# Optimization experiments

Measured on AMD Instinct MI355X. Metric: run time of the kernel, lower is better.

The kernel has to match this reference:

```python
import jax, jax.numpy as jnp
import numpy as np

N_MELS = 80
LSTM_DIM = 1024
ATT_DIM = 128
ENC_DIM = 512
PRENET = 256
LOC_FILT = 32
LOC_K = 31


def _lstm_step(x, h, c, k, r, b):
    z = x @ k + h @ r + b  # [B, 4*LSTM_DIM], keras gate order i,f,g,o
    i, f, g, o = jnp.split(z, 4, axis=-1)
    c2 = jax.nn.sigmoid(f) * c + jax.nn.sigmoid(i) * jnp.tanh(g)
    h2 = jax.nn.sigmoid(o) * jnp.tanh(c2)
    return h2, c2


def setup_inputs() -> dict:
    key = jax.random.key(0)
    ks = jax.random.split(key, 24)
    s = 0.05
    B, Tm, T = 32, 200, 400
    inp = {
        'memory': jax.random.normal(ks[0], (B, Tm, ENC_DIM), jnp.float32),
        'decoder_inputs': jax.random.normal(ks[1], (B, N_MELS, T), jnp.float32),
        # Prenet (2 dense+relu layers)
        'prenet_w0': jax.random.normal(ks[2], (N_MELS, PRENET)) * s,
        'prenet_b0': jnp.zeros((PRENET,)),
        'prenet_w1': jax.random.normal(ks[3], (PRENET, PRENET)) * s,
        'prenet_b1': jnp.zeros((PRENET,)),
        # LSTM 1: input = prenet(256) + context(512) = 768
        'lstm1_k': jax.random.normal(ks[4], (PRENET + ENC_DIM, 4 * LSTM_DIM)) * s,
        'lstm1_r': jax.random.normal(ks[5], (LSTM_DIM, 4 * LSTM_DIM)) * s,
        'lstm1_b': jnp.zeros((4 * LSTM_DIM,)),
        # LSTM 2: input = att_hidden(1024) + context(512) = 1536
        'lstm2_k': jax.random.normal(ks[6], (LSTM_DIM + ENC_DIM, 4 * LSTM_DIM)) * s,
        'lstm2_r': jax.random.normal(ks[7], (LSTM_DIM, 4 * LSTM_DIM)) * s,
        'lstm2_b': jnp.zeros((4 * LSTM_DIM,)),
        # Attention
        'wq': jax.random.normal(ks[8], (LSTM_DIM, ATT_DIM)) * s,
        'wm': jax.random.normal(ks[9], (ENC_DIM, ATT_DIM)) * s,
        'v': jax.random.normal(ks[10], (ATT_DIM,)) * s,
        'loc_conv': jax.random.normal(ks[11], (LOC_K, 2, LOC_FILT)) * s,  # WIO
        'loc_dense': jax.random.normal(ks[12], (LOC_FILT, ATT_DIM)) * s,
        # Projections: input = dec_hidden(1024) + context(512) = 1536
        'frame_w': jax.random.normal(ks[13], (LSTM_DIM + ENC_DIM, N_MELS)) * s,
        'frame_b': jnp.zeros((N_MELS,)),
        'stop_w': jax.random.normal(ks[14], (LSTM_DIM + ENC_DIM, 1)) * s,
        'stop_b': jnp.zeros((1,)),
    }
    return inp


def reference(memory, decoder_inputs, prenet_w0, prenet_b0, prenet_w1, prenet_b1,
              lstm1_k, lstm1_r, lstm1_b, lstm2_k, lstm2_r, lstm2_b,
              wq, wm, v, loc_conv, loc_dense, frame_w, frame_b, stop_w, stop_b):
    B, Tm, _ = memory.shape
    T = decoder_inputs.shape[2]

    # parse_decoder_inputs: [B, n_mels, T] -> [T, B, n_mels]; prepend go frame
    dec_in = jnp.transpose(decoder_inputs, (2, 0, 1))
    dec_in = jnp.concatenate([jnp.zeros((1, B, N_MELS), memory.dtype), dec_in], axis=0)
    # Prenet (dropout identity in inference mode)
    x = jax.nn.relu(dec_in @ prenet_w0 + prenet_b0)
    x = jax.nn.relu(x @ prenet_w1 + prenet_b1)  # [T+1, B, 256]

    processed_memory = jnp.tanh(memory @ wm)  # [B, Tm, ATT_DIM]

    def step(carry, xt):
        att_h, att_c, dec_h, dec_c, att_w, att_w_cum, att_ctx = carry
        # Attention RNN
        cell_in = jnp.concatenate([xt, att_ctx], axis=-1)
        att_h, att_c = _lstm_step(cell_in, att_h, att_c, lstm1_k, lstm1_r, lstm1_b)
        # Location-sensitive attention
        awc = jnp.stack([att_w, att_w_cum], axis=-1)  # [B, Tm, 2]
        loc = jax.lax.conv_general_dilated(awc, loc_conv, (1,), 'SAME',
                                           dimension_numbers=('NWC', 'WIO', 'NWC'))
        loc = jnp.tanh(loc @ loc_dense)  # [B, Tm, ATT_DIM]
        q = jnp.tanh(att_h @ wq)[:, None, :]  # [B, 1, ATT_DIM]
        energies = jnp.tanh(q + loc + processed_memory) @ v  # [B, Tm]
        att_w = jax.nn.softmax(energies, axis=1)
        att_ctx = jnp.einsum('bt,btd->bd', att_w, memory)  # [B, ENC_DIM]
        att_w_cum = att_w_cum + att_w
        # Decoder RNN
        dec_in2 = jnp.concatenate([att_h, att_ctx], axis=-1)
        dec_h, dec_c = _lstm_step(dec_in2, dec_h, dec_c, lstm2_k, lstm2_r, lstm2_b)
        dhac = jnp.concatenate([dec_h, att_ctx], axis=-1)
        mel = dhac @ frame_w + frame_b  # [B, n_mels]
        gate = jax.nn.sigmoid(dhac @ stop_w + stop_b)[:, 0]  # [B]
        carry = (att_h, att_c, dec_h, dec_c, att_w, att_w_cum, att_ctx)
        return carry, (mel, gate, att_w)

    z = jnp.zeros((B, LSTM_DIM), memory.dtype)
    zw = jnp.zeros((B, Tm), memory.dtype)
    zc = jnp.zeros((B, ENC_DIM), memory.dtype)
    carry0 = (z, z, z, z, zw, zw, zc)
    _, (mels, gates, aligns) = jax.lax.scan(step, carry0, x[:T])

    # parse_decoder_outputs
    mel_outputs = jnp.transpose(mels, (1, 2, 0))      # [B, n_mels, T]
    gate_outputs = jnp.transpose(gates, (1, 0))       # [B, T]
    alignments = jnp.transpose(aligns, (1, 0, 2))     # [B, T, Tm]
    return mel_outputs, gate_outputs, alignments
```

## Files before the change

### kernel.cpp

```cpp
#include <hip/hip_runtime.h>
#include <math.h>

#define TSTEPS 400

#define KSP1 7
#define KSP2 8

#define OFF_XPRE  0u
#define OFF_PM    1638400u
#define OFF_IN1T  2457600u
#define OFF_IN2T  2506752u
#define OFF_ZP1   2588672u
#define OFF_ZP2   3506176u
#define OFF_CTXP  4554752u
#define OFF_H2B   4620288u
#define OFF_C1    4685824u
#define OFF_C2    4718592u
#define OFF_ATTW  4751360u
#define OFF_CUM   4757760u
#define WS_FLOATS 4764160u

#define OUT_GATE  1024000
#define OUT_ALIGN 1036800

__device__ __forceinline__ float sigf(float x)   { return 1.f / (1.f + __expf(-x)); }
__device__ __forceinline__ float tanhf_(float x) { return 1.f - 2.f / (__expf(2.f*x) + 1.f); }

__global__ void __launch_bounds__(256) prenet_kernel(
    const float* __restrict__ dec, const float* __restrict__ w0, const float* __restrict__ b0,
    const float* __restrict__ w1, const float* __restrict__ b1, float* __restrict__ ws)
{
    __shared__ float s_in[80];
    __shared__ float s_h0[256];
    int t = blockIdx.x, b = blockIdx.y, tid = threadIdx.x;
    if (tid < 80) s_in[tid] = (t == 0) ? 0.f : dec[b*32000 + tid*400 + (t-1)];
    __syncthreads();
    float s = b0[tid];
    for (int m = 0; m < 80; ++m) s = fmaf(s_in[m], w0[m*256 + tid], s);
    s_h0[tid] = fmaxf(s, 0.f);
    __syncthreads();
    float s2 = b1[tid];
    for (int k = 0; k < 256; ++k) s2 = fmaf(s_h0[k], w1[k*256 + tid], s2);
    float v = fmaxf(s2, 0.f);
    unsigned u = __float_as_uint(v);
    u += 0x7fffu + ((u >> 16) & 1u);
    ((unsigned short*)(ws + OFF_XPRE))[(size_t)t*8192 + tid*32 + b] = (unsigned short)(u >> 16);
}

__global__ void __launch_bounds__(128) pmem_kernel(
    const float* __restrict__ mp, const float* __restrict__ wm, float* __restrict__ ws)
{
    int t = blockIdx.x, b = blockIdx.y, a = threadIdx.x;
    const float* mrow = mp + (b*200 + t)*512;
    float s = 0.f;
    for (int d = 0; d < 512; ++d) s = fmaf(mrow[d], wm[d*128 + a], s);
    ws[OFF_PM + (b*200 + t)*128 + a] = tanhf_(s);
}

__global__ void __launch_bounds__(256) zero_kernel(float* __restrict__ ws)
{
    int gid = blockIdx.x*256 + threadIdx.x, gsz = gridDim.x*256;
    for (int i = gid; i < 49152; i += gsz) ws[OFF_IN1T + i] = 0.f;
    for (int i = gid; i < 81920; i += gsz) ws[OFF_IN2T + i] = 0.f;
    for (int i = gid; i < 32768; i += gsz) { ws[OFF_C1 + i] = 0.f; ws[OFF_C2 + i] = 0.f; }
    for (int i = gid; i < 65536; i += gsz) { ws[OFF_CTXP + i] = 0.f; ws[OFF_H2B + i] = 0.f; }
    for (int i = gid; i < 6400;  i += gsz) { ws[OFF_ATTW + i] = 0.f; ws[OFF_CUM + i] = 0.f; }
}

#define FMA8(XA, XB, W)                                                                               \
    a[0].x = fmaf(XA.x, W.x, a[0].x); a[0].y = fmaf(XA.x, W.y, a[0].y); a[0].z = fmaf(XA.x, W.z, a[0].z); a[0].w = fmaf(XA.x, W.w, a[0].w); \
    a[1].x = fmaf(XA.y, W.x, a[1].x); a[1].y = fmaf(XA.y, W.y, a[1].y); a[1].z = fmaf(XA.y, W.z, a[1].z); a[1].w = fmaf(XA.y, W.w, a[1].w); \
    a[2].x = fmaf(XA.z, W.x, a[2].x); a[2].y = fmaf(XA.z, W.y, a[2].y); a[2].z = fmaf(XA.z, W.z, a[2].z); a[2].w = fmaf(XA.z, W.w, a[2].w); \
    a[3].x = fmaf(XA.w, W.x, a[3].x); a[3].y = fmaf(XA.w, W.y, a[3].y); a[3].z = fmaf(XA.w, W.z, a[3].z); a[3].w = fmaf(XA.w, W.w, a[3].w); \
    a[4].x = fmaf(XB.x, W.x, a[4].x); a[4].y = fmaf(XB.x, W.y, a[4].y); a[4].z = fmaf(XB.x, W.z, a[4].z); a[4].w = fmaf(XB.x, W.w, a[4].w); \
    a[5].x = fmaf(XB.y, W.x, a[5].x); a[5].y = fmaf(XB.y, W.y, a[5].y); a[5].z = fmaf(XB.y, W.z, a[5].z); a[5].w = fmaf(XB.y, W.w, a[5].w); \
    a[6].x = fmaf(XB.z, W.x, a[6].x); a[6].y = fmaf(XB.z, W.y, a[6].y); a[6].z = fmaf(XB.z, W.z, a[6].z); a[6].w = fmaf(XB.z, W.w, a[6].w); \
    a[7].x = fmaf(XB.w, W.x, a[7].x); a[7].y = fmaf(XB.w, W.y, a[7].y); a[7].z = fmaf(XB.w, W.z, a[7].z); a[7].w = fmaf(XB.w, W.w, a[7].w)

__global__ void __launch_bounds__(512, 4) kernel_P1(
    const float* __restrict__ l1k, const float* __restrict__ l1r,
    const float* __restrict__ l2k, const float* __restrict__ l2r,
    float* __restrict__ ws, int t)
{
    __shared__ float s_lds[12288];
    const int tid = threadIdx.x, bid = blockIdx.x;
    const int jq = tid & 31, bgrp = (tid >> 5) & 3, ksub = tid >> 7;
    const int b0 = bgrp*8;
    float4 a[8];
#pragma unroll
    for (int i = 0; i < 8; ++i) a[i] = make_float4(0.f, 0.f, 0.f, 0.f);

    if (bid < 224) {
        if (t >= TSTEPS) return;
        const int colgrp = bid & 31, ksp = bid >> 5;
        const int j = colgrp*128 + jq*4;

        if (ksp == 0) {
            const uint4* src = (const uint4*)((const unsigned short*)(ws + OFF_XPRE) + (size_t)t*8192);
            for (int i = tid; i < 1024; i += 512) {
                uint4 p = src[i];
                float* d = s_lds + i*8;
                d[0] = __uint_as_float(p.x << 16); d[1] = __uint_as_float(p.x & 0xffff0000u);
                d[2] = __uint_as_float(p.y << 16); d[3] = __uint_as_float(p.y & 0xffff0000u);
                d[4] = __uint_as_float(p.z << 16); d[5] = __uint_as_float(p.z & 0xffff0000u);
                d[6] = __uint_as_float(p.w << 16); d[7] = __uint_as_float(p.w & 0xffff0000u);
            }
        } else {
            const float4* src = (const float4*)(ws + OFF_IN1T - 8192 + (size_t)ksp*256*32);
            float4* dst = (float4*)s_lds;
            for (int i = tid; i < 2048; i += 512) dst[i] = src[i];
        }
        __syncthreads();

        const int kl0 = ksub*64;
        const int kg0 = ksp*256 + kl0;
        const float* wb = (kg0 < 768) ? (l1k + (size_t)kg0*4096 + j)
                                      : (l1r + (size_t)(kg0 - 768)*4096 + j);
        float4 wbuf[4];
#pragma unroll
        for (int i = 0; i < 4; ++i) wbuf[i] = *(const float4*)(wb + (size_t)i*4096);
        for (int kk = 0; kk < 60; kk += 4) {
            float4 wn[4];
#pragma unroll
            for (int i = 0; i < 4; ++i) wn[i] = *(const float4*)(wb + (size_t)(kk + 4 + i)*4096);
#pragma unroll
            for (int i = 0; i < 4; ++i) {
                const float* xp = s_lds + (kl0 + kk + i)*32 + b0;
                float4 xa = *(const float4*)xp;
                float4 xb = *(const float4*)(xp + 4);
                FMA8(xa, xb, wbuf[i]);
            }
#pragma unroll
            for (int i = 0; i < 4; ++i) wbuf[i] = wn[i];
        }
#pragma unroll
        for (int i = 0; i < 4; ++i) {
            const float* xp = s_lds + (kl0 + 60 + i)*32 + b0;
            float4 xa = *(const float4*)xp;
            float4 xb = *(const float4*)(xp + 4);
            FMA8(xa, xb, wbuf[i]);
        }

        __syncthreads();
        if (ksub) {
#pragma unroll
            for (int i = 0; i < 8; ++i)
                *(float4*)(s_lds + (ksub-1)*4096 + (b0 + i)*128 + jq*4) = a[i];
        }
        __syncthreads();
        if (!ksub) {
            float* zp1 = ws + OFF_ZP1;
#pragma unroll
            for (int i = 0; i < 8; ++i) {
                float4 r0 = *(const float4*)(s_lds +         (b0 + i)*128 + jq*4);
                float4 r1 = *(const float4*)(s_lds +  4096 + (b0 + i)*128 + jq*4);
                float4 r2 = *(const float4*)(s_lds +  8192 + (b0 + i)*128 + jq*4);
                a[i].x += r0.x + r1.x + r2.x; a[i].y += r0.y + r1.y + r2.y;
                a[i].z += r0.z + r1.z + r2.z; a[i].w += r0.w + r1.w + r2.w;
                *(float4*)(zp1 + (size_t)(ksp*32 + b0 + i)*4096 + j) = a[i];
            }
        }
    } else {
        if (t < 1 || t > TSTEPS) return;
        const int g = bid - 224;
        const int colgrp = g & 31, ksp = g >> 5;
        const int j = colgrp*128 + jq*4;

        {
            const float4* src = (const float4*)(ws + OFF_IN2T + (size_t)ksp*320*32);
            float4* dst = (float4*)s_lds;
            for (int i = tid; i < 2560; i += 512) dst[i] = src[i];
        }
        __syncthreads();

        const int kl0 = ksub*80;
        const int kg0 = ksp*320 + kl0;
        float4 wbuf[4];
#pragma unroll
        for (int i = 0; i < 4; ++i) {
            int kg = kg0 + i;
            const float* wr = (kg < 1536) ? (l2k + (size_t)kg*4096)
                                          : (l2r + (size_t)(kg - 1536)*4096);
            wbuf[i] = *(const float4*)(wr + j);
        }
        for (int kk = 0; kk < 76; kk += 4) {
            float4 wn[4];
#pragma unroll
            for (int i = 0; i < 4; ++i) {
                int kg = kg0 + kk + 4 + i;
                const float* wr = (kg < 1536) ? (l2k + (size_t)kg*4096)
                                              : (l2r + (size_t)(kg - 1536)*4096);
                wn[i] = *(const float4*)(wr + j);
            }
#pragma unroll
            for (int i = 0; i < 4; ++i) {
                const float* xp = s_lds + (kl0 + kk + i)*32 + b0;
                float4 xa = *(const float4*)xp;
                float4 xb = *(const float4*)(xp + 4);
                FMA8(xa, xb, wbuf[i]);
            }
#pragma unroll
            for (int i = 0; i < 4; ++i) wbuf[i] = wn[i];
        }
#pragma unroll
        for (int i = 0; i < 4; ++i) {
            const float* xp = s_lds + (kl0 + 76 + i)*32 + b0;
            float4 xa = *(const float4*)xp;
            float4 xb = *(const float4*)(xp + 4);
            FMA8(xa, xb, wbuf[i]);
        }

        __syncthreads();
        if (ksub) {
#pragma unroll
            for (int i = 0; i < 8; ++i)
                *(float4*)(s_lds + (ksub-1)*4096 + (b0 + i)*128 + jq*4) = a[i];
        }
        __syncthreads();
        if (!ksub) {
            float* zp2 = ws + OFF_ZP2;
#pragma unroll
            for (int i = 0; i < 8; ++i) {
                float4 r0 = *(const float4*)(s_lds +         (b0 + i)*128 + jq*4);
                float4 r1 = *(const float4*)(s_lds +  4096 + (b0 + i)*128 + jq*4);
                float4 r2 = *(const float4*)(s_lds +  8192 + (b0 + i)*128 + jq*4);
                a[i].x += r0.x + r1.x + r2.x; a[i].y += r0.y + r1.y + r2.y;
                a[i].z += r0.z + r1.z + r2.z; a[i].w += r0.w + r1.w + r2.w;
                *(float4*)(zp2 + (size_t)(ksp*32 + b0 + i)*4096 + j) = a[i];
            }
        }
    }
}

__global__ void __launch_bounds__(1024) kernel_P2(
    const float* __restrict__ mp, const float* __restrict__ l1b, const float* __restrict__ l2b,
    const float* __restrict__ wq, const float* __restrict__ vvec,
    const float* __restrict__ lconv, const float* __restrict__ ldense,
    const float* __restrict__ fw, const float* __restrict__ fb,
    const float* __restrict__ sw, const float* __restrict__ sb,
    float* __restrict__ ws, float* __restrict__ out, int t)
{
    __shared__ float s_attw[200], s_cum[200];
    __shared__ float s_hid[1024], s_q[128], s_ex[200], s_den[1];
    __shared__ float s_co[200*33];
    __shared__ float s_red[1024];
    const int tid = threadIdx.x, bid = blockIdx.x;
    float* in1m = ws + OFF_IN1T - 8192;
    float* in2T = ws + OFF_IN2T;
    float* zp1  = ws + OFF_ZP1;
    float* zp2  = ws + OFF_ZP2;
    float* ctxp = ws + OFF_CTXP;
    float* h2bb = ws + OFF_H2B;
    float* c1a  = ws + OFF_C1;
    float* c2a  = ws + OFF_C2;
    float* attw = ws + OFF_ATTW;
    float* cum  = ws + OFF_CUM;
    const float* pm = ws + OFF_PM;

    if (bid < 32) {
        if (t >= TSTEPS) return;
        const int b = bid;
        {
            int u = tid;
            float zi = l1b[u], zf = l1b[1024+u], zg = l1b[2048+u], zo = l1b[3072+u];
#pragma unroll
            for (int kc = 0; kc < KSP1; ++kc) {
                const float* zr = zp1 + (size_t)(kc*32 + b)*4096;
                zi += zr[u]; zf += zr[1024+u]; zg += zr[2048+u]; zo += zr[3072+u];
            }
            float c = sigf(zf)*c1a[b*1024+u] + sigf(zi)*tanhf_(zg);
            float h = sigf(zo)*tanhf_(c);
            c1a[b*1024+u] = c;
            s_hid[u] = h;
            in1m[(768+u)*32 + b] = h;
            in2T[u*32 + b] = h;
        }
        if (tid < 200) { s_attw[tid] = attw[b*200 + tid]; s_cum[tid] = cum[b*200 + tid]; }
        __syncthreads();
        {
            int a = tid & 127, kq = tid >> 7;
            float s = 0.f;
            for (int k = kq*128; k < kq*128 + 128; ++k)
                s = fmaf(s_hid[k], wq[k*128 + a], s);
            s_red[tid] = s;
        }
        __syncthreads();
        if (tid < 128) {
            float s = 0.f;
#pragma unroll
            for (int q = 0; q < 8; ++q) s += s_red[q*128 + tid];
            s_q[tid] = tanhf_(s);
        }
        for (int idx = tid; idx < 6400; idx += 1024) {
            int tl = idx >> 5, f = idx & 31;
            float s = 0.f;
            for (int dw = 0; dw < 31; ++dw) {
                int tg = tl - 15 + dw;
                if (tg >= 0 && tg < 200) {
                    s = fmaf(s_attw[tg], lconv[(dw*2+0)*32 + f], s);
                    s = fmaf(s_cum[tg],  lconv[(dw*2+1)*32 + f], s);
                }
            }
            s_co[tl*33 + f] = s;
        }
        __syncthreads();
        if (tid < 800) {
            int tl = tid >> 2, aq = tid & 3;
            const float* pmrow = pm + (b*200 + tl)*128;
            float e = 0.f;
            for (int a = aq*32; a < aq*32 + 32; ++a) {
                float s = 0.f;
#pragma unroll
                for (int f = 0; f < 32; ++f) s = fmaf(s_co[tl*33 + f], ldense[f*128 + a], s);
                float en = tanhf_(s_q[a] + tanhf_(s) + pmrow[a]);
                e = fmaf(en, vvec[a], e);
            }
            e += __shfl_xor(e, 1, 4);
            e += __shfl_xor(e, 2, 4);
            if (aq == 0) s_ex[tl] = __expf(e);
        }
        __syncthreads();
        if (tid < 64) {
            float s = 0.f;
            for (int i = tid; i < 200; i += 64) s += s_ex[i];
            for (int off = 32; off; off >>= 1) s += __shfl_down(s, off, 64);
            if (tid == 0) s_den[0] = s;
        }
        __syncthreads();
        if (tid < 200) {
            float w = s_ex[tid] / s_den[0];
            s_attw[tid] = w;
            attw[b*200 + tid] = w;
            cum[b*200 + tid] = s_cum[tid] + w;
            out[OUT_ALIGN + (b*400 + t)*200 + tid] = w;
        }
        __syncthreads();
        {
            int d = tid & 511, th = tid >> 9;
            float s = 0.f;
            for (int tt = th*100; tt < th*100 + 100; ++tt)
                s = fmaf(s_attw[tt], mp[(b*200 + tt)*512 + d], s);
            s_red[tid] = s;
        }
        __syncthreads();
        if (tid < 512) {
            float cv = s_red[tid] + s_red[512 + tid];
            ctxp[(size_t)(t & 3)*16384 + b*512 + tid] = cv;
            in1m[(256 + tid)*32 + b] = cv;
            in2T[(1024 + tid)*32 + b] = cv;
        }
    } else if (bid < 64) {
        if (t < 1 || t > TSTEPS) return;
        const int b = bid - 32, t1 = t - 1;
        float* h2b = h2bb + (size_t)(t1 & 1)*32768;
        int u = tid;
        float zi = l2b[u], zf = l2b[1024+u], zg = l2b[2048+u], zo = l2b[3072+u];
#pragma unroll
        for (int kc = 0; kc < KSP2; ++kc) {
            const float* zr = zp2 + (size_t)(kc*32 + b)*4096;
            zi += zr[u]; zf += zr[1024+u]; zg += zr[2048+u]; zo += zr[3072+u];
        }
        float c = sigf(zf)*c2a[b*1024+u] + sigf(zi)*tanhf_(zg);
        float h = sigf(zo)*tanhf_(c);
        c2a[b*1024+u] = c;
        in2T[(1536+u)*32 + b] = h;
        h2b[u*32 + b] = h;
    } else if (bid < 74) {
        if (t < 2) return;
        const int t2 = t - 2;
        const int mc = bid - 64;
        const int m_l = tid & 7, b = (tid >> 3) & 31, kh = tid >> 8;
        const int m = mc*8 + m_l;
        const float* cp = ctxp + (size_t)((t2 & 3)*32 + b)*512;
        const float* h2b = h2bb + (size_t)(t2 & 1)*32768;
        float s = 0.f;
        for (int k = kh*384; k < kh*384 + 384; ++k) {
            float dv = (k < 1024) ? h2b[k*32 + b] : cp[k - 1024];
            s = fmaf(dv, fw[k*80 + m], s);
        }
        s_red[tid] = s;
        __syncthreads();
        if (tid < 256) {
            float v4 = s_red[tid] + s_red[256+tid] + s_red[512+tid] + s_red[768+tid];
            int b2 = tid >> 3, m2 = mc*8 + (tid & 7);
            out[(b2*80 + m2)*400 + t2] = v4 + fb[m2];
        }
    } else {
        if (t < 2) return;
        const int t2 = t - 2;
        const int b = tid >> 5, kh = tid & 31;
        const float* cp = ctxp + (size_t)((t2 & 3)*32 + b)*512;
        const float* h2b = h2bb + (size_t)(t2 & 1)*32768;
        float s = 0.f;
        for (int k = kh*48; k < kh*48 + 48; ++k) {
            float dv = (k < 1024) ? h2b[k*32 + b] : cp[k - 1024];
            s = fmaf(dv, sw[k], s);
        }
        s_red[b*32 + kh] = s;
        __syncthreads();
        if (tid < 32) {
            float z = 0.f;
#pragma unroll
            for (int i = 0; i < 32; ++i) z += s_red[tid*32 + i];
            out[OUT_GATE + tid*400 + t2] = sigf(z + sb[0]);
        }
    }
}

extern "C" void kernel_launch(void* const* d_in, const int* in_sizes, int n_in,
                              void* d_out, int out_size, void* d_ws, size_t ws_size,
                              hipStream_t stream) {
    (void)in_sizes; (void)n_in; (void)out_size;
    const float* mp    = (const float*)d_in[0];
    const float* dec   = (const float*)d_in[1];
    const float* pw0   = (const float*)d_in[2];
    const float* pb0   = (const float*)d_in[3];
    const float* pw1   = (const float*)d_in[4];
    const float* pb1   = (const float*)d_in[5];
    const float* l1k   = (const float*)d_in[6];
    const float* l1r   = (const float*)d_in[7];
    const float* l1b   = (const float*)d_in[8];
    const float* l2k   = (const float*)d_in[9];
    const float* l2r   = (const float*)d_in[10];
    const float* l2b   = (const float*)d_in[11];
    const float* wq    = (const float*)d_in[12];
    const float* wm    = (const float*)d_in[13];
    const float* vvec  = (const float*)d_in[14];
    const float* lconv = (const float*)d_in[15];
    const float* ldns  = (const float*)d_in[16];
    const float* fw    = (const float*)d_in[17];
    const float* fb    = (const float*)d_in[18];
    const float* sw    = (const float*)d_in[19];
    const float* sb    = (const float*)d_in[20];
    float* ws  = (float*)d_ws;
    float* out = (float*)d_out;

    if (ws_size < (size_t)WS_FLOATS * sizeof(float)) return;

    prenet_kernel<<<dim3(400, 32), 256, 0, stream>>>(dec, pw0, pb0, pw1, pb1, ws);
    pmem_kernel  <<<dim3(200, 32), 128, 0, stream>>>(mp, wm, ws);
    zero_kernel  <<<256, 256, 0, stream>>>(ws);

    for (int t = 0; t <= TSTEPS; ++t) {
        kernel_P1<<<480, 512, 0, stream>>>(l1k, l1r, l2k, l2r, ws, t);
        kernel_P2<<<75, 1024, 0, stream>>>(mp, l1b, l2b, wq, vvec, lconv, ldns,
                                           fw, fb, sw, sb, ws, out, t);
    }
    kernel_P2<<<75, 1024, 0, stream>>>(mp, l1b, l2b, wq, vvec, lconv, ldns,
                                       fw, fb, sw, sb, ws, out, TSTEPS + 1);
}
```

Baseline: 75.90 ms.

## Move mel/gate projections into P1 and rebalance GEMM k-split per thread

Moves the frame and stop projections out of the serial attention/LSTM kernel P2 and into the wide P1 kernel as extra blocks, so they run alongside the LSTM gate GEMMs and P2 becomes shorter on the critical path. The P1 GEMM is reorganised from a 4-way k-split with 8 batch rows per thread to a 2-way k-split with 4 batch rows and 8-deep weight prefetch, which shrinks the LDS reduction and changes register pressure. It also adds unroll pragmas to several P2 loops. The projection blocks now run at step t in P1 instead of after P2, which depends on buffer parity timing staying correct.

After: 110.3 ms. +45.3%, slower.

```diff
diff --git a/kernel.cpp b/kernel.cpp
--- a/kernel.cpp
+++ b/kernel.cpp
@@ -67,167 +67,197 @@
     for (int i = gid; i < 6400;  i += gsz) { ws[OFF_ATTW + i] = 0.f; ws[OFF_CUM + i] = 0.f; }
 }
 
-#define FMA8(XA, XB, W)                                                                               \
-    a[0].x = fmaf(XA.x, W.x, a[0].x); a[0].y = fmaf(XA.x, W.y, a[0].y); a[0].z = fmaf(XA.x, W.z, a[0].z); a[0].w = fmaf(XA.x, W.w, a[0].w); \
-    a[1].x = fmaf(XA.y, W.x, a[1].x); a[1].y = fmaf(XA.y, W.y, a[1].y); a[1].z = fmaf(XA.y, W.z, a[1].z); a[1].w = fmaf(XA.y, W.w, a[1].w); \
-    a[2].x = fmaf(XA.z, W.x, a[2].x); a[2].y = fmaf(XA.z, W.y, a[2].y); a[2].z = fmaf(XA.z, W.z, a[2].z); a[2].w = fmaf(XA.z, W.w, a[2].w); \
-    a[3].x = fmaf(XA.w, W.x, a[3].x); a[3].y = fmaf(XA.w, W.y, a[3].y); a[3].z = fmaf(XA.w, W.z, a[3].z); a[3].w = fmaf(XA.w, W.w, a[3].w); \
-    a[4].x = fmaf(XB.x, W.x, a[4].x); a[4].y = fmaf(XB.x, W.y, a[4].y); a[4].z = fmaf(XB.x, W.z, a[4].z); a[4].w = fmaf(XB.x, W.w, a[4].w); \
-    a[5].x = fmaf(XB.y, W.x, a[5].x); a[5].y = fmaf(XB.y, W.y, a[5].y); a[5].z = fmaf(XB.y, W.z, a[5].z); a[5].w = fmaf(XB.y, W.w, a[5].w); \
-    a[6].x = fmaf(XB.z, W.x, a[6].x); a[6].y = fmaf(XB.z, W.y, a[6].y); a[6].z = fmaf(XB.z, W.z, a[6].z); a[6].w = fmaf(XB.z, W.w, a[6].w); \
-    a[7].x = fmaf(XB.w, W.x, a[7].x); a[7].y = fmaf(XB.w, W.y, a[7].y); a[7].z = fmaf(XB.w, W.z, a[7].z); a[7].w = fmaf(XB.w, W.w, a[7].w)
+#define FMA4(X, W)                                                                                    \
+    a[0].x = fmaf(X.x, W.x, a[0].x); a[0].y = fmaf(X.x, W.y, a[0].y); a[0].z = fmaf(X.x, W.z, a[0].z); a[0].w = fmaf(X.x, W.w, a[0].w); \
+    a[1].x = fmaf(X.y, W.x, a[1].x); a[1].y = fmaf(X.y, W.y, a[1].y); a[1].z = fmaf(X.y, W.z, a[1].z); a[1].w = fmaf(X.y, W.w, a[1].w); \
+    a[2].x = fmaf(X.z, W.x, a[2].x); a[2].y = fmaf(X.z, W.y, a[2].y); a[2].z = fmaf(X.z, W.z, a[2].z); a[2].w = fmaf(X.z, W.w, a[2].w); \
+    a[3].x = fmaf(X.w, W.x, a[3].x); a[3].y = fmaf(X.w, W.y, a[3].y); a[3].z = fmaf(X.w, W.z, a[3].z); a[3].w = fmaf(X.w, W.w, a[3].w)
 
 __global__ void __launch_bounds__(512, 4) kernel_P1(
     const float* __restrict__ l1k, const float* __restrict__ l1r,
     const float* __restrict__ l2k, const float* __restrict__ l2r,
-    float* __restrict__ ws, int t)
+    const float* __restrict__ fw, const float* __restrict__ fb,
+    const float* __restrict__ sw, const float* __restrict__ sb,
+    float* __restrict__ ws, float* __restrict__ out, int t)
 {
-    __shared__ float s_lds[12288];
+    __shared__ float s_lds[10240];
     const int tid = threadIdx.x, bid = blockIdx.x;
-    const int jq = tid & 31, bgrp = (tid >> 5) & 3, ksub = tid >> 7;
-    const int b0 = bgrp*8;
-    float4 a[8];
-#pragma unroll
-    for (int i = 0; i < 8; ++i) a[i] = make_float4(0.f, 0.f, 0.f, 0.f);
-
-    if (bid < 224) {
-        if (t >= TSTEPS) return;
-        const int colgrp = bid & 31, ksp = bid >> 5;
-        const int j = colgrp*128 + jq*4;
-
-        if (ksp == 0) {
-            const uint4* src = (const uint4*)((const unsigned short*)(ws + OFF_XPRE) + (size_t)t*8192);
-            for (int i = tid; i < 1024; i += 512) {
-                uint4 p = src[i];
-                float* d = s_lds + i*8;
-                d[0] = __uint_as_float(p.x << 16); d[1] = __uint_as_float(p.x & 0xffff0000u);
-                d[2] = __uint_as_float(p.y << 16); d[3] = __uint_as_float(p.y & 0xffff0000u);
-                d[4] = __uint_as_float(p.z << 16); d[5] = __uint_as_float(p.z & 0xffff0000u);
-                d[6] = __uint_as_float(p.w << 16); d[7] = __uint_as_float(p.w & 0xffff0000u);
+
+    if (bid < 480) {
+        const int jq = tid & 31, bgrp = (tid >> 5) & 7, ksub = tid >> 8;
+        const int b0 = bgrp*4;
+        float4 a[4];
+#pragma unroll
+        for (int i = 0; i < 4; ++i) a[i] = make_float4(0.f, 0.f, 0.f, 0.f);
+
+        if (bid < 224) {
+            if (t >= TSTEPS) return;
+            const int colgrp = bid & 31, ksp = bid >> 5;
+            const int j = colgrp*128 + jq*4;
+
+            if (ksp == 0) {
+                const uint4* src = (const uint4*)((const unsigned short*)(ws + OFF_XPRE) + (size_t)t*8192);
+                for (int i = tid; i < 1024; i += 512) {
+                    uint4 p = src[i];
+                    float* d = s_lds + i*8;
+                    d[0] = __uint_as_float(p.x << 16); d[1] = __uint_as_float(p.x & 0xffff0000u);
+                    d[2] = __uint_as_float(p.y << 16); d[3] = __uint_as_float(p.y & 0xffff0000u);
+                    d[4] = __uint_as_float(p.z << 16); d[5] = __uint_as_float(p.z & 0xffff0000u);
+                    d[6] = __uint_as_float(p.w << 16); d[7] = __uint_as_float(p.w & 0xffff0000u);
+                }
+            } else {
+                const float4* src = (const float4*)(ws + OFF_IN1T - 8192 + (size_t)ksp*256*32);
+                float4* dst = (float4*)s_lds;
+                for (int i = tid; i < 2048; i += 512) dst[i] = src[i];
+            }
+            __syncthreads();
+
+            const int kl0 = ksub*128;
+            const int kg0 = ksp*256 + kl0;
+            const float* wb = (ksp < 3) ? (l1k + (size_t)kg0*4096 + j)
+                                        : (l1r + (size_t)(kg0 - 768)*4096 + j);
+            const float* xb = s_lds + kl0*32 + b0;
+            float4 wc[8], wn[8];
+#pragma unroll
+            for (int i = 0; i < 8; ++i) wc[i] = *(const float4*)(wb + (size_t)i*4096);
+            for (int kk = 0; kk < 120; kk += 8) {
+#pragma unroll
+                for (int i = 0; i < 8; ++i) wn[i] = *(const float4*)(wb + (size_t)(kk + 8 + i)*4096);
+#pragma unroll
+                for (int i = 0; i < 8; ++i) {
+                    float4 x = *(const float4*)(xb + (kk + i)*32);
+                    FMA4(x, wc[i]);
+                }
+#pragma unroll
+                for (int i = 0; i < 8; ++i) wc[i] = wn[i];
+            }
+#pragma unroll
+            for (int i = 0; i < 8; ++i) {
+                float4 x = *(const float4*)(xb + (120 + i)*32);
+                FMA4(x, wc[i]);
+            }
+
+            __syncthreads();
+            if (ksub) {
+#pragma unroll
+                for (int i = 0; i < 4; ++i)
+                    *(float4*)(s_lds + (b0 + i)*128 + jq*4) = a[i];
+            }
+            __syncthreads();
+            if (!ksub) {
+                float* zp1 = ws + OFF_ZP1;
+#pragma unroll
+                for (int i = 0; i < 4; ++i) {
+                    float4 r = *(const float4*)(s_lds + (b0 + i)*128 + jq*4);
+                    a[i].x += r.x; a[i].y += r.y; a[i].z += r.z; a[i].w += r.w;
+                    *(float4*)(zp1 + (size_t)(ksp*32 + b0 + i)*4096 + j) = a[i];
+                }
             }
         } else {
-            const float4* src = (const float4*)(ws + OFF_IN1T - 8192 + (size_t)ksp*256*32);
-            float4* dst = (float4*)s_lds;
-            for (int i = tid; i < 2048; i += 512) dst[i] = src[i];
-        }
-        __syncthreads();
-
-        const int kl0 = ksub*64;
-        const int kg0 = ksp*256 + kl0;
-        const float* wb = (kg0 < 768) ? (l1k + (size_t)kg0*4096 + j)
-                                      : (l1r + (size_t)(kg0 - 768)*4096 + j);
-        float4 wbuf[4];
-#pragma unroll
-        for (int i = 0; i < 4; ++i) wbuf[i] = *(const float4*)(wb + (size_t)i*4096);
-        for (int kk = 0; kk < 60; kk += 4) {
-            float4 wn[4];
-#pragma unroll
-            for (int i = 0; i < 4; ++i) wn[i] = *(const float4*)(wb + (size_t)(kk + 4 + i)*4096);
-#pragma unroll
-            for (int i = 0; i < 4; ++i) {
-                const float* xp = s_lds + (kl0 + kk + i)*32 + b0;
-                float4 xa = *(const float4*)xp;
-                float4 xb = *(const float4*)(xp + 4);
-                FMA8(xa, xb, wbuf[i]);
-            }
-#pragma unroll
-            for (int i = 0; i < 4; ++i) wbuf[i] = wn[i];
-        }
-#pragma unroll
-        for (int i = 0; i < 4; ++i) {
-            const float* xp = s_lds + (kl0 + 60 + i)*32 + b0;
-            float4 xa = *(const float4*)xp;
-            float4 xb = *(const float4*)(xp + 4);
-            FMA8(xa, xb, wbuf[i]);
-        }
-
-        __syncthreads();
-        if (ksub) {
-#pragma unroll
-            for (int i = 0; i < 8; ++i)
-                *(float4*)(s_lds + (ksub-1)*4096 + (b0 + i)*128 + jq*4) = a[i];
-        }
-        __syncthreads();
-        if (!ksub) {
-            float* zp1 = ws + OFF_ZP1;
+            if (t < 1 || t > TSTEPS) return;
+            const int g = bid - 224;
+            const int colgrp = g & 31, ksp = g >> 5;
+            const int j = colgrp*128 + jq*4;
+
+            {
+                const float4* src = (const float4*)(ws + OFF_IN2T + (size_t)ksp*320*32);
+                float4* dst = (float4*)s_lds;
+                for (int i = tid; i < 2560; i += 512) dst[i] = src[i];
+            }
+            __syncthreads();
+
+            const int kl0 = ksub*160;
+            const int kg0 = ksp*320 + kl0;
+            const float* xb = s_lds + kl0*32 + b0;
+            float4 wc[8], wn[8];
 #pragma unroll
             for (int i = 0; i < 8; ++i) {
-                float4 r0 = *(const float4*)(s_lds +         (b0 + i)*128 + jq*4);
-                float4 r1 = *(const float4*)(s_lds +  4096 + (b0 + i)*128 + jq*4);
-                float4 r2 = *(const float4*)(s_lds +  8192 + (b0 + i)*128 + jq*4);
-                a[i].x += r0.x + r1.x + r2.x; a[i].y += r0.y + r1.y + r2.y;
-                a[i].z += r0.z + r1.z + r2.z; a[i].w += r0.w + r1.w + r2.w;
-                *(float4*)(zp1 + (size_t)(ksp*32 + b0 + i)*4096 + j) = a[i];
-            }
-        }
-    } else {
-        if (t < 1 || t > TSTEPS) return;
-        const int g = bid - 224;
-        const int colgrp = g & 31, ksp = g >> 5;
-        const int j = colgrp*128 + jq*4;
-
-        {
-            const float4* src = (const float4*)(ws + OFF_IN2T + (size_t)ksp*320*32);
-            float4* dst = (float4*)s_lds;
-            for (int i = tid; i < 2560; i += 512) dst[i] = src[i];
-        }
-        __syncthreads();
-
-        const int kl0 = ksub*80;
-        const int kg0 = ksp*320 + kl0;
-        float4 wbuf[4];
-#pragma unroll
-        for (int i = 0; i < 4; ++i) {
-            int kg = kg0 + i;
-            const float* wr = (kg < 1536) ? (l2k + (size_t)kg*4096)
-                                          : (l2r + (size_t)(kg - 1536)*4096);
-            wbuf[i] = *(const float4*)(wr + j);
-        }
-        for (int kk = 0; kk < 76; kk += 4) {
-            float4 wn[4];
-#pragma unroll
-            for (int i = 0; i < 4; ++i) {
-                int kg = kg0 + kk + 4 + i;
+                int kg = kg0 + i;
                 const float* wr = (kg < 1536) ? (l2k + (size_t)kg*4096)
                                               : (l2r + (size_t)(kg - 1536)*4096);
-                wn[i] = *(const float4*)(wr + j);
-            }
-#pragma unroll
-            for (int i = 0; i < 4; ++i) {
-                const float* xp = s_lds + (kl0 + kk + i)*32 + b0;
-                float4 xa = *(const float4*)xp;
-                float4 xb = *(const float4*)(xp + 4);
-                FMA8(xa, xb, wbuf[i]);
-            }
-#pragma unroll
-            for (int i = 0; i < 4; ++i) wbuf[i] = wn[i];
-        }
-#pragma unroll
-        for (int i = 0; i < 4; ++i) {
-            const float* xp = s_lds + (kl0 + 76 + i)*32 + b0;
-            float4 xa = *(const float4*)xp;
-            float4 xb = *(const float4*)(xp + 4);
-            FMA8(xa, xb, wbuf[i]);
-        }
-
-        __syncthreads();
-        if (ksub) {
-#pragma unroll
-            for (int i = 0; i < 8; ++i)
-                *(float4*)(s_lds + (ksub-1)*4096 + (b0 + i)*128 + jq*4) = a[i];
-        }
-        __syncthreads();
-        if (!ksub) {
-            float* zp2 = ws + OFF_ZP2;
+                wc[i] = *(const float4*)(wr + j);
+            }
+            for (int kk = 0; kk < 152; kk += 8) {
+#pragma unroll
+                for (int i = 0; i < 8; ++i) {
+                    int kg = kg0 + kk + 8 + i;
+                    const float* wr = (kg < 1536) ? (l2k + (size_t)kg*4096)
+                                                  : (l2r + (size_t)(kg - 1536)*4096);
+                    wn[i] = *(const float4*)(wr + j);
+                }
+#pragma unroll
+                for (int i = 0; i < 8; ++i) {
+                    float4 x = *(const float4*)(xb + (kk + i)*32);
+                    FMA4(x, wc[i]);
+                }
+#pragma unroll
+                for (int i = 0; i < 8; ++i) wc[i] = wn[i];
+            }
 #pragma unroll
             for (int i = 0; i < 8; ++i) {
-                float4 r0 = *(const float4*)(s_lds +         (b0 + i)*128 + jq*4);
-                float4 r1 = *(const float4*)(s_lds +  4096 + (b0 + i)*128 + jq*4);
-                float4 r2 = *(const float4*)(s_lds +  8192 + (b0 + i)*128 + jq*4);
-                a[i].x += r0.x + r1.x + r2.x; a[i].y += r0.y + r1.y + r2.y;
-                a[i].z += r0.z + r1.z + r2.z; a[i].w += r0.w + r1.w + r2.w;
-                *(float4*)(zp2 + (size_t)(ksp*32 + b0 + i)*4096 + j) = a[i];
-            }
+                float4 x = *(const float4*)(xb + (152 + i)*32);
+                FMA4(x, wc[i]);
+            }
+
+            __syncthreads();
+            if (ksub) {
+#pragma unroll
+                for (int i = 0; i < 4; ++i)
+                    *(float4*)(s_lds + (b0 + i)*128 + jq*4) = a[i];
+            }
+            __syncthreads();
+            if (!ksub) {
+                float* zp2 = ws + OFF_ZP2;
+#pragma unroll
+                for (int i = 0; i < 4; ++i) {
+                    float4 r = *(const float4*)(s_lds + (b0 + i)*128 + jq*4);
+                    a[i].x += r.x; a[i].y += r.y; a[i].z += r.z; a[i].w += r.w;
+                    *(float4*)(zp2 + (size_t)(ksp*32 + b0 + i)*4096 + j) = a[i];
+                }
+            }
+        }
+    } else if (bid < 520) {
+        if (t < 2 || t > TSTEPS + 1) return;
+        const int t2 = t - 2;
+        const int mc = bid - 480;
+        const int m_l = tid & 1, b = (tid >> 1) & 31, kh = tid >> 6;
+        const int m = mc*2 + m_l;
+        const float* cp  = ws + OFF_CTXP + (size_t)((t2 & 3)*32 + b)*512;
+        const float* h2b = ws + OFF_H2B + (size_t)(t2 & 1)*32768;
+        float s = 0.f;
+#pragma unroll 8
+        for (int k = kh*192; k < kh*192 + 192; ++k) {
+            float dv = (k < 1024) ? h2b[k*32 + b] : cp[k - 1024];
+            s = fmaf(dv, fw[k*80 + m], s);
+        }
+        s_lds[tid] = s;
+        __syncthreads();
+        if (tid < 64) {
+            float v = 0.f;
+#pragma unroll
+            for (int kh2 = 0; kh2 < 8; ++kh2) v += s_lds[kh2*64 + tid];
+            int b2 = tid >> 1, m2 = mc*2 + (tid & 1);
+            out[(b2*80 + m2)*400 + t2] = v + fb[m2];
+        }
+    } else {
+        if (t < 2 || t > TSTEPS + 1) return;
+        const int t2 = t - 2;
+        const int b = tid >> 4, kh = tid & 15;
+        const float* cp  = ws + OFF_CTXP + (size_t)((t2 & 3)*32 + b)*512;
+        const float* h2b = ws + OFF_H2B + (size_t)(t2 & 1)*32768;
+        float s = 0.f;
+#pragma unroll 8
+        for (int k = kh*96; k < kh*96 + 96; ++k) {
+            float dv = (k < 1024) ? h2b[k*32 + b] : cp[k - 1024];
+            s = fmaf(dv, sw[k], s);
+        }
+        s_lds[tid] = s;
+        __syncthreads();
+        if (tid < 32) {
+            float z = 0.f;
+#pragma unroll
+            for (int i = 0; i < 16; ++i) z += s_lds[tid*16 + i];
+            out[OUT_GATE + tid*400 + t2] = sigf(z + sb[0]);
         }
     }
 }
@@ -236,8 +266,6 @@
     const float* __restrict__ mp, const float* __restrict__ l1b, const float* __restrict__ l2b,
     const float* __restrict__ wq, const float* __restrict__ vvec,
     const float* __restrict__ lconv, const float* __restrict__ ldense,
-    const float* __restrict__ fw, const float* __restrict__ fb,
-    const float* __restrict__ sw, const float* __restrict__ sb,
     float* __restrict__ ws, float* __restrict__ out, int t)
 {
     __shared__ float s_attw[200], s_cum[200];
@@ -280,6 +308,7 @@
         {
             int a = tid & 127, kq = tid >> 7;
             float s = 0.f;
+#pragma unroll 8
             for (int k = kq*128; k < kq*128 + 128; ++k)
                 s = fmaf(s_hid[k], wq[k*128 + a], s);
             s_red[tid] = s;
@@ -308,6 +337,7 @@
             int tl = tid >> 2, aq = tid & 3;
             const float* pmrow = pm + (b*200 + tl)*128;
             float e = 0.f;
+#pragma unroll 2
             for (int a = aq*32; a < aq*32 + 32; ++a) {
                 float s = 0.f;
 #pragma unroll
@@ -338,6 +368,7 @@
         {
             int d = tid & 511, th = tid >> 9;
             float s = 0.f;
+#pragma unroll 10
             for (int tt = th*100; tt < th*100 + 100; ++tt)
                 s = fmaf(s_attw[tt], mp[(b*200 + tt)*512 + d], s);
             s_red[tid] = s;
@@ -349,7 +380,7 @@
             in1m[(256 + tid)*32 + b] = cv;
             in2T[(1024 + tid)*32 + b] = cv;
         }
-    } else if (bid < 64) {
+    } else {
         if (t < 1 || t > TSTEPS) return;
         const int b = bid - 32, t1 = t - 1;
         float* h2b = h2bb + (size_t)(t1 & 1)*32768;
@@ -365,45 +396,6 @@
         c2a[b*1024+u] = c;
         in2T[(1536+u)*32 + b] = h;
         h2b[u*32 + b] = h;
-    } else if (bid < 74) {
-        if (t < 2) return;
-        const int t2 = t - 2;
-        const int mc = bid - 64;
-        const int m_l = tid & 7, b = (tid >> 3) & 31, kh = tid >> 8;
-        const int m = mc*8 + m_l;
-        const float* cp = ctxp + (size_t)((t2 & 3)*32 + b)*512;
-        const float* h2b = h2bb + (size_t)(t2 & 1)*32768;
-        float s = 0.f;
-        for (int k = kh*384; k < kh*384 + 384; ++k) {
-            float dv = (k < 1024) ? h2b[k*32 + b] : cp[k - 1024];
-            s = fmaf(dv, fw[k*80 + m], s);
-        }
-        s_red[tid] = s;
-        __syncthreads();
-        if (tid < 256) {
-            float v4 = s_red[tid] + s_red[256+tid] + s_red[512+tid] + s_red[768+tid];
-            int b2 = tid >> 3, m2 = mc*8 + (tid & 7);
-            out[(b2*80 + m2)*400 + t2] = v4 + fb[m2];
-        }
-    } else {
-        if (t < 2) return;
-        const int t2 = t - 2;
-        const int b = tid >> 5, kh = tid & 31;
-        const float* cp = ctxp + (size_t)((t2 & 3)*32 + b)*512;
-        const float* h2b = h2bb + (size_t)(t2 & 1)*32768;
-        float s = 0.f;
-        for (int k = kh*48; k < kh*48 + 48; ++k) {
-            float dv = (k < 1024) ? h2b[k*32 + b] : cp[k - 1024];
-            s = fmaf(dv, sw[k], s);
-        }
-        s_red[b*32 + kh] = s;
-        __syncthreads();
-        if (tid < 32) {
-            float z = 0.f;
-#pragma unroll
-            for (int i = 0; i < 32; ++i) z += s_red[tid*32 + i];
-            out[OUT_GATE + tid*400 + t2] = sigf(z + sb[0]);
-        }
     }
 }
 
@@ -442,10 +434,8 @@
     zero_kernel  <<<256, 256, 0, stream>>>(ws);
 
     for (int t = 0; t <= TSTEPS; ++t) {
-        kernel_P1<<<480, 512, 0, stream>>>(l1k, l1r, l2k, l2r, ws, t);
-        kernel_P2<<<75, 1024, 0, stream>>>(mp, l1b, l2b, wq, vvec, lconv, ldns,
-                                           fw, fb, sw, sb, ws, out, t);
+        kernel_P1<<<521, 512, 0, stream>>>(l1k, l1r, l2k, l2r, fw, fb, sw, sb, ws, out, t);
+        kernel_P2<<<64, 1024, 0, stream>>>(mp, l1b, l2b, wq, vvec, lconv, ldns, ws, out, t);
     }
-    kernel_P2<<<75, 1024, 0, stream>>>(mp, l1b, l2b, wq, vvec, lconv, ldns,
-                                       fw, fb, sw, sb, ws, out, TSTEPS + 1);
-}
+    kernel_P1<<<521, 512, 0, stream>>>(l1k, l1r, l2k, l2r, fw, fb, sw, sb, ws, out, TSTEPS + 1);
+}
```
